# Optimization experiments

Hardware: AMD Instinct MI355X
Metric: run time of the kernel (lower is better)

## Reference

```python
import jax, jax.numpy as jnp
import numpy as np

B, S, H, V = 16, 128, 512, 50000
N, R = 5, 2          # mem_size, read_heads
Wd = H               # memory cell width
EPS = 1e-6
XI_SIZES = [R * Wd, R, Wd, 1, Wd, Wd, R, 1, 1, 3 * R]
XI = int(np.sum(XI_SIZES))  # 2573


def oneplus(x):
    return 1.0 + jax.nn.softplus(x)


def content_weight(M, k, beta):
    # M: [B,N,Wd], k: [B,R,Wd], beta: [B,R] -> [B,R,N]
    Mn = M / (jnp.linalg.norm(M, axis=-1, keepdims=True) + EPS)
    kn = k / (jnp.linalg.norm(k, axis=-1, keepdims=True) + EPS)
    sim = jnp.einsum('brw,bnw->brn', kn, Mn)
    return jax.nn.softmax(beta[:, :, None] * sim, axis=-1)


def setup_inputs() -> dict:
    key = jax.random.key(0)
    ks = jax.random.split(key, 8)
    emb = jax.random.normal(ks[0], (V, H), jnp.float32) * 0.02
    emb = emb.at[0].set(0.0)  # PAD row
    return {
        'source': jax.random.randint(ks[1], (B, S), 0, V),
        'source_lengths': jax.random.randint(ks[2], (B,), 1, S + 1),
        'emb': emb,
        'W_ih': jax.random.normal(ks[3], (4 * H, H + R * Wd), jnp.float32) * 0.02,
        'W_hh': jax.random.normal(ks[4], (4 * H, H), jnp.float32) * 0.02,
        'b_lstm': jnp.zeros((4 * H,), jnp.float32),
        'W_int': jax.random.normal(ks[5], (H, XI), jnp.float32) * 0.02,
        'b_int': jnp.zeros((XI,), jnp.float32),
        'W_out': jax.random.normal(ks[6], (H + R * Wd, H), jnp.float32) * 0.02,
        'b_out': jnp.zeros((H,), jnp.float32),
    }


def dnc_forward(source, emb, W_ih, W_hh, b_lstm, W_int, b_int, W_out, b_out):
    x_emb = emb[source]  # [B,S,H] embedding lookup
    splits = np.cumsum(XI_SIZES)[:-1]
    eye = jnp.eye(N, dtype=jnp.float32)

    def step(carry, x_t):
        h, c, M, u, p, L, wr, ww, r = carry
        # LSTM controller: input = [embedded token; read vectors]
        xin = jnp.concatenate([x_t, r.reshape(-1, R * Wd)], axis=-1)
        gates = xin @ W_ih.T + h @ W_hh.T + b_lstm
        i_, f_, g_, o_ = jnp.split(gates, 4, axis=-1)
        c = jax.nn.sigmoid(f_) * c + jax.nn.sigmoid(i_) * jnp.tanh(g_)
        h = jax.nn.sigmoid(o_) * jnp.tanh(c)
        # interface vector
        xi = h @ W_int + b_int
        (rk, rb, wk, wb, e, v, fg, ga, gw, pi) = jnp.split(xi, splits, axis=-1)
        rk = rk.reshape(-1, R, Wd)
        rb = oneplus(rb)                       # [B,R]
        wb = oneplus(wb)                       # [B,1]
        e = jax.nn.sigmoid(e)                  # [B,Wd]
        fg = jax.nn.sigmoid(fg)                # [B,R]
        ga = jax.nn.sigmoid(ga)                # [B,1]
        gw = jax.nn.sigmoid(gw)                # [B,1]
        pi = jax.nn.softmax(pi.reshape(-1, R, 3), axis=-1)
        # usage / retention
        psi = jnp.prod(1.0 - fg[:, :, None] * wr, axis=1)        # [B,N]
        u = (u + ww - u * ww) * psi
        # allocation weighting (sort-based, irregular access)
        phi = jnp.argsort(u, axis=-1)
        u_s = jnp.take_along_axis(u, phi, axis=-1)
        excl = jnp.concatenate([jnp.ones_like(u_s[:, :1]), jnp.cumprod(u_s, axis=-1)[:, :-1]], axis=-1)
        a_s = (1.0 - u_s) * excl
        a = jnp.take_along_axis(a_s, jnp.argsort(phi, axis=-1), axis=-1)
        # write weighting
        cw = content_weight(M, wk[:, None, :], wb)[:, 0]         # [B,N]
        ww = gw * (ga * a + (1.0 - ga) * cw)
        # memory write
        M = M * (1.0 - ww[:, :, None] * e[:, None, :]) + ww[:, :, None] * v[:, None, :]
        # temporal link matrix + precedence
        L = (1.0 - ww[:, :, None] - ww[:, None, :]) * L + ww[:, :, None] * p[:, None, :]
        L = L * (1.0 - eye)
        p = (1.0 - ww.sum(-1, keepdims=True)) * p + ww
        # read weightings
        fw = jnp.einsum('bij,brj->bri', L, wr)
        bw = jnp.einsum('bji,brj->bri', L, wr)
        cr = content_weight(M, rk, rb)                           # [B,R,N]
        wr = pi[..., 0:1] * bw + pi[..., 1:2] * cr + pi[..., 2:3] * fw
        r = jnp.einsum('brn,bnw->brw', wr, M)                    # [B,R,Wd]
        out_t = jnp.concatenate([h, r.reshape(-1, R * Wd)], axis=-1) @ W_out + b_out
        return (h, c, M, u, p, L, wr, ww, r), out_t

    z = jnp.zeros
    init = (z((B, H)), z((B, H)), z((B, N, Wd)), z((B, N)), z((B, N)),
            z((B, N, N)), z((B, R, N)), z((B, N)), z((B, R, Wd)))
    (h, c, *_), outs = jax.lax.scan(step, init, jnp.swapaxes(x_emb, 0, 1))
    return jnp.swapaxes(outs, 0, 1), h, c


def reference(source, source_lengths, emb, W_ih, W_hh, b_lstm, W_int, b_int, W_out, b_out):
    outputs, h, c = dnc_forward(source, emb, W_ih, W_hh, b_lstm, W_int, b_int, W_out, b_out)
    return outputs, (h, c)
```

## Files before the change

kernel.cpp:

```cpp
#include <hip/hip_runtime.h>
#include <math.h>

#define EPSC 1e-6f
#define NBLK 256
#define GBLK 64

#define OFF_H     0u
#define OFF_R     16384u
#define OFF_FLAGS 32768u
#define OFF_GO    40960u
#define OFF_XF    49152u
#define OFF_RF    57344u
#define STATE_END 58368u
#define OFF_XI    58368u
#define OFF_GX    107520u
#define OFF_HR    4301824u

typedef float f32x4 __attribute__((ext_vector_type(4)));

__device__ __forceinline__ float sigmf(float x) { return 1.0f / (1.0f + expf(-x)); }
__device__ __forceinline__ float oneplusf(float x) {
    return 1.0f + fmaxf(x, 0.0f) + log1pf(expf(-fabsf(x)));
}

__device__ __forceinline__ void gst(float* p, float v) {
    __hip_atomic_store((unsigned*)p, __float_as_uint(v),
                       __ATOMIC_RELAXED, __HIP_MEMORY_SCOPE_AGENT);
}

__device__ __forceinline__ void ld6g(
    f32x4& h0, f32x4& h1,
    f32x4& r0, f32x4& r1, f32x4& r2, f32x4& r3,
    const float* ph, const float* pr)
{
    asm volatile(
        "global_load_dwordx4 %0, %6, off sc0 sc1\n\t"
        "global_load_dwordx4 %1, %6, off offset:1024 sc0 sc1\n\t"
        "global_load_dwordx4 %2, %7, off sc0 sc1\n\t"
        "global_load_dwordx4 %3, %7, off offset:1024 sc0 sc1\n\t"
        "global_load_dwordx4 %4, %7, off offset:2048 sc0 sc1\n\t"
        "global_load_dwordx4 %5, %7, off offset:3072 sc0 sc1\n\t"
        "s_waitcnt vmcnt(0)"
        : "=&v"(h0), "=&v"(h1), "=&v"(r0), "=&v"(r1), "=&v"(r2), "=&v"(r3)
        : "v"(ph), "v"(pr)
        : "memory");
}

__device__ __forceinline__ void ld2h(f32x4& d0, f32x4& d1, const float* p)
{
    asm volatile(
        "global_load_dwordx4 %0, %2, off sc0 sc1\n\t"
        "global_load_dwordx4 %1, %2, off offset:1024 sc0 sc1\n\t"
        "s_waitcnt vmcnt(0)"
        : "=&v"(d0), "=&v"(d1)
        : "v"(p)
        : "memory");
}

__device__ __forceinline__ void cld3(
    f32x4& d0, f32x4& d1, f32x4& d2,
    const float* p0, const float* p1, const float* p2)
{
    asm volatile(
        "global_load_dwordx4 %0, %3, off sc0 sc1\n\t"
        "global_load_dwordx4 %1, %4, off sc0 sc1\n\t"
        "global_load_dwordx4 %2, %5, off sc0 sc1\n\t"
        "s_waitcnt vmcnt(0)"
        : "=&v"(d0), "=&v"(d1), "=&v"(d2)
        : "v"(p0), "v"(p1), "v"(p2)
        : "memory");
}

__device__ __forceinline__ void gsync(unsigned* flags, unsigned* go, unsigned gen,
                                      int bi, int bl, int g, int tid)
{
    __builtin_amdgcn_s_waitcnt(0);
    __syncthreads();
    if (tid == 0)
        __hip_atomic_store(&flags[bi * 32], gen, __ATOMIC_RELAXED, __HIP_MEMORY_SCOPE_AGENT);
    if (bl == 0) {
        if (tid < GBLK) {
            unsigned v;
            do {
                v = __hip_atomic_load(&flags[(g * GBLK + tid) * 32], __ATOMIC_RELAXED,
                                      __HIP_MEMORY_SCOPE_AGENT);
                if (v < gen) __builtin_amdgcn_s_sleep(1);
            } while (v < gen);
        }
        __syncthreads();
        if (tid < GBLK)
            __hip_atomic_store(&go[(g * GBLK + tid) * 32], gen, __ATOMIC_RELAXED,
                               __HIP_MEMORY_SCOPE_AGENT);
    }
    if (tid == 0) {
        unsigned v;
        do {
            v = __hip_atomic_load(&go[bi * 32], __ATOMIC_RELAXED, __HIP_MEMORY_SCOPE_AGENT);
            if (v < gen) __builtin_amdgcn_s_sleep(1);
        } while (v < gen);
    }
    __syncthreads();
}

template <int K>
__device__ __forceinline__ void blk_reduce(float* v, float (*s_red)[20],
                                           float* outp, int tid)
{
#pragma unroll
    for (int i = 0; i < K; i++) {
        float x = v[i];
        for (int o = 32; o > 0; o >>= 1) x += __shfl_down(x, o, 64);
        if ((tid & 63) == 0) s_red[tid >> 6][i] = x;
    }
    __syncthreads();
    if (tid < K) outp[tid] = s_red[0][tid] + s_red[1][tid] + s_red[2][tid] + s_red[3][tid];
    __syncthreads();
}

__global__ __launch_bounds__(256, 1) void k_main(
    const float* __restrict__ W_ih, const float* __restrict__ W_hh,
    const float* __restrict__ W_int, const float* __restrict__ b_int,
    const float* __restrict__ gx, float* __restrict__ hbuf,
    float* __restrict__ rbuf, float* __restrict__ xib,
    float* __restrict__ hr, float* __restrict__ out,
    unsigned* __restrict__ flags, unsigned* __restrict__ go,
    unsigned* __restrict__ xf, unsigned* __restrict__ rf)
{
    const int tid = threadIdx.x;
    const int bi  = blockIdx.x;
    const int g   = bi >> 6;
    const int bl  = bi & 63;
    const int bg0 = g * 4;

    __shared__ __align__(16) float big_u[6656];
    __shared__ __align__(16) float s_xi[3072];
    __shared__ float s_part[512];
    __shared__ float s_tot[128];
    __shared__ float c_s[32];
    __shared__ __align__(16) float s_M[5][520];
    __shared__ float st_u[5], st_p[5], st_L[25], st_wr[10], st_ww[5];
    __shared__ float s_red[4][20];
    __shared__ float s_rb[2], s_wb, s_fg[2], s_ga, s_gw, s_pi[2][3];
    __shared__ float s_wrold[2][5], s_uu[5], s_a[5], s_wwn[5];
    __shared__ float s_pold[5], s_Lnew[25];
    __shared__ float s_zw[5], s_z[2][5], s_fw[2][5], s_bw[2][5];
    __shared__ float s_dotA[11], s_dotB[17], s_wrnew[2][5];

    if (tid < 32) c_s[tid] = 0.f;
    if (bl < 4) {
        for (int i = tid; i < 5 * 520; i += 256) (&s_M[0][0])[i] = 0.f;
        if (tid < 5)  { st_u[tid] = 0.f; st_p[tid] = 0.f; st_ww[tid] = 0.f; }
        if (tid < 25) st_L[tid] = 0.f;
        if (tid < 10) st_wr[tid] = 0.f;
    }
    __syncthreads();

    const int cq = tid & 7;
    const int ks = tid >> 3;
    const int jcol = bl * 8 + cq;
    const int b4 = tid >> 6, sg = tid & 63;

#pragma unroll 1
    for (int t = 0; t < 128; t++) {
        const float* h_in  = hbuf + (t & 1) * 8192;
        float*       h_out = hbuf + ((t + 1) & 1) * 8192;

        float gxv = 0.f;
        if (tid < 128) {
            int c = tid & 31, b = tid >> 5;
            int col = (c >> 3) * 512 + bl * 8 + (c & 7);
            gxv = gx[((size_t)t * 16 + bg0 + b) * 2048 + col];
        }
        if (tid < 4) {
            unsigned v;
            do {
                v = __hip_atomic_load(&rf[(bg0 + tid) * 32], __ATOMIC_RELAXED,
                                      __HIP_MEMORY_SCOPE_AGENT);
                if (v < (unsigned)t) __builtin_amdgcn_s_sleep(4);
            } while (v < (unsigned)t);
        }
        __syncthreads();

        {
            const float* ph = h_in + (bg0 + b4) * 512 + sg * 4;
            const float* pr = rbuf + (bg0 + b4) * 1024 + sg * 4;
            f32x4 h0, h1, r0, r1, r2, r3;
            ld6g(h0, h1, r0, r1, r2, r3, ph, pr);
#define STG(kk, D) { int k = (kk); int cc = k / 48; \
                     *(f32x4*)&big_u[b4 * 1664 + cc * 52 + (k - cc * 48)] = D; }
            STG(sg * 4 + 0 * 256, h0)        STG(sg * 4 + 1 * 256, h1)
            STG(512 + sg * 4 + 0 * 256, r0)  STG(512 + sg * 4 + 1 * 256, r1)
            STG(512 + sg * 4 + 2 * 256, r2)  STG(512 + sg * 4 + 3 * 256, r3)
#undef STG
        }
        __syncthreads();

        float acc[4][4];
#pragma unroll
        for (int g_ = 0; g_ < 4; g_++)
#pragma unroll
            for (int b = 0; b < 4; b++) acc[g_][b] = 0.f;
#pragma unroll
        for (int i = 0; i < 12; i++) {
            int kg = ks * 48 + i * 4;
            f32x4 w[4];
#pragma unroll
            for (int g_ = 0; g_ < 4; g_++) {
                const float* wp = (kg < 512)
                    ? W_hh + (size_t)(g_ * 512 + jcol) * 512 + kg
                    : W_ih + (size_t)(g_ * 512 + jcol) * 1536 + kg;
                w[g_] = *(const f32x4*)wp;
            }
#pragma unroll
            for (int b = 0; b < 4; b++) {
                f32x4 xv = *(const f32x4*)&big_u[b * 1664 + ks * 52 + i * 4];
#pragma unroll
                for (int g_ = 0; g_ < 4; g_++) {
                    acc[g_][b] = fmaf(w[g_][0], xv[0], acc[g_][b]);
                    acc[g_][b] = fmaf(w[g_][1], xv[1], acc[g_][b]);
                    acc[g_][b] = fmaf(w[g_][2], xv[2], acc[g_][b]);
                    acc[g_][b] = fmaf(w[g_][3], xv[3], acc[g_][b]);
                }
            }
        }
#pragma unroll
        for (int g_ = 0; g_ < 4; g_++)
#pragma unroll
            for (int b = 0; b < 4; b++) {
                float x = acc[g_][b];
                x += __shfl_xor(x, 8, 64);
                x += __shfl_xor(x, 16, 64);
                x += __shfl_xor(x, 32, 64);
                acc[g_][b] = x;
            }
        {
            int wv = tid >> 6;
            if ((tid & 63) < 8) {
#pragma unroll
                for (int g_ = 0; g_ < 4; g_++)
#pragma unroll
                    for (int b = 0; b < 4; b++)
                        s_part[((wv * 4 + g_) * 8 + cq) * 4 + b] = acc[g_][b];
            }
        }
        __syncthreads();
        if (tid < 128) {
            int c = tid & 31, b = tid >> 5;
            int g_ = c >> 3, jq = c & 7;
            float tot = gxv;
#pragma unroll
            for (int w = 0; w < 4; w++)
                tot += s_part[((w * 4 + g_) * 8 + jq) * 4 + b];
            s_tot[c * 4 + b] = tot;
        }
        __syncthreads();
        if (tid < 32) {
            int jl = tid & 7, b = tid >> 3;
            float gi  = s_tot[(0 * 8 + jl) * 4 + b];
            float gf  = s_tot[(1 * 8 + jl) * 4 + b];
            float gg  = s_tot[(2 * 8 + jl) * 4 + b];
            float go_ = s_tot[(3 * 8 + jl) * 4 + b];
            float cc = sigmf(gf) * c_s[jl * 4 + b] + sigmf(gi) * tanhf(gg);
            float hh = sigmf(go_) * tanhf(cc);
            c_s[jl * 4 + b] = cc;
            int j = bl * 8 + jl;
            int bgl = bg0 + b;
            gst(h_out + bgl * 512 + j, hh);
            hr[((size_t)t * 16 + bgl) * 1536 + j] = hh;
            if (t == 127) {
                out[1048576 + bgl * 512 + j] = hh;
                out[1048576 + 8192 + bgl * 512 + j] = cc;
            }
        }
        gsync(flags, go, (unsigned)(t + 1), bi, bl, g, tid);

        {
            {
                const float* ph = h_out + (bg0 + b4) * 512 + sg * 4;
                f32x4 e0, e1;
                ld2h(e0, e1, ph);
#define STX(j, E) { int k = sg * 4 + (j) * 256; \
                    *(f32x4*)&big_u[b4 * 592 + (k >> 5) * 36 + (k & 31)] = E; }
                STX(0, e0) STX(1, e1)
#undef STX
            }
            __syncthreads();
            const int ql  = tid & 15;
            const int kcl = tid >> 4;
#pragma unroll 1
            for (int p = 0; p < 3; p++) {
                if (p == 2 && bl >= 33) break;
                int q0 = p * 1024 + bl * 16;
                int q  = q0 + ql;
                int qc = (q < 2573) ? q : 2572;
                float wxr[32];
#pragma unroll
                for (int i = 0; i < 32; i++)
                    wxr[i] = W_int[(size_t)(kcl * 32 + i) * 2573 + qc];
                float ax[4];
#pragma unroll
                for (int b = 0; b < 4; b++) ax[b] = 0.f;
#pragma unroll
                for (int b = 0; b < 4; b++) {
                    const f32x4* hp = (const f32x4*)&big_u[b * 592 + kcl * 36];
#pragma unroll
                    for (int i4 = 0; i4 < 8; i4++) {
                        f32x4 hv = hp[i4];
                        ax[b] = fmaf(wxr[i4 * 4 + 0], hv[0], ax[b]);
                        ax[b] = fmaf(wxr[i4 * 4 + 1], hv[1], ax[b]);
                        ax[b] = fmaf(wxr[i4 * 4 + 2], hv[2], ax[b]);
                        ax[b] = fmaf(wxr[i4 * 4 + 3], hv[3], ax[b]);
                    }
                }
#pragma unroll
                for (int b = 0; b < 4; b++) {
                    float x = ax[b];
                    x += __shfl_xor(x, 16, 64);
                    x += __shfl_xor(x, 32, 64);
                    ax[b] = x;
                }
                {
                    int wv = tid >> 6;
                    if ((tid & 63) < 16) {
#pragma unroll
                        for (int b = 0; b < 4; b++)
                            s_part[(wv * 16 + ql) * 4 + b] = ax[b];
                    }
                }
                __syncthreads();
                if (tid < 64) {
                    int q_l = tid >> 2, b = tid & 3;
                    int qq = q0 + q_l;
                    if (qq < 2573) {
                        float v = b_int[qq];
#pragma unroll
                        for (int w = 0; w < 4; w++)
                            v += s_part[(w * 16 + q_l) * 4 + b];
                        gst(&xib[(bg0 + b) * 3072 + qq], v);
                    }
                }
                __syncthreads();
            }
        }
        __builtin_amdgcn_s_waitcnt(0);
        __syncthreads();
        if (tid == 0)
            __hip_atomic_store(&xf[bi * 32], (unsigned)(t + 1),
                               __ATOMIC_RELAXED, __HIP_MEMORY_SCOPE_AGENT);

        if (bl < 4) {
            const int bg = bg0 + bl;
            if (tid < GBLK) {
                unsigned v;
                do {
                    v = __hip_atomic_load(&xf[(g * GBLK + tid) * 32], __ATOMIC_RELAXED,
                                          __HIP_MEMORY_SCOPE_AGENT);
                    if (v < (unsigned)(t + 1)) __builtin_amdgcn_s_sleep(2);
                } while (v < (unsigned)(t + 1));
            }
            __syncthreads();
            {
                const float* xs = xib + bg * 3072;
                f32x4 d0, d1, d2;
                cld3(d0, d1, d2,
                     xs + (tid + 0) * 4, xs + (tid + 256) * 4, xs + (tid + 512) * 4);
                *(f32x4*)&s_xi[(tid + 0) * 4]   = d0;
                *(f32x4*)&s_xi[(tid + 256) * 4] = d1;
                *(f32x4*)&s_xi[(tid + 512) * 4] = d2;
            }
            __syncthreads();
            const float* xb = s_xi;

            if (tid == 0) {
                s_wb = oneplusf(xb[1538]);
                s_ga = sigmf(xb[2565]);
                s_gw = sigmf(xb[2566]);
            }
            if (tid == 1 || tid == 2) {
                int rr = tid - 1;
                s_rb[rr] = oneplusf(xb[1024 + rr]);
                s_fg[rr] = sigmf(xb[2563 + rr]);
                float z0 = xb[2567 + rr * 3], z1 = xb[2568 + rr * 3], z2 = xb[2569 + rr * 3];
                float mx = fmaxf(z0, fmaxf(z1, z2));
                float e0 = expf(z0 - mx), e1 = expf(z1 - mx), e2 = expf(z2 - mx);
                float s = e0 + e1 + e2;
                s_pi[rr][0] = e0 / s; s_pi[rr][1] = e1 / s; s_pi[rr][2] = e2 / s;
            }
            if (tid >= 32 && tid < 42) { int i = tid - 32; s_wrold[i / 5][i % 5] = st_wr[i]; }
            if (tid >= 64 && tid < 69) { s_pold[tid - 64] = st_p[tid - 64]; }
            __syncthreads();
            if (tid < 5) {
                float psi = (1.f - s_fg[0] * s_wrold[0][tid]) * (1.f - s_fg[1] * s_wrold[1][tid]);
                float un = (st_u[tid] + st_ww[tid] - st_u[tid] * st_ww[tid]) * psi;
                s_uu[tid] = un; st_u[tid] = un;
            }
            __syncthreads();
            if (tid < 5) {
                float excl = 1.f;
#pragma unroll
                for (int m2 = 0; m2 < 5; m2++) {
                    bool before = (s_uu[m2] < s_uu[tid]) || (s_uu[m2] == s_uu[tid] && m2 < tid);
                    if (before) excl *= s_uu[m2];
                }
                s_a[tid] = (1.f - s_uu[tid]) * excl;
            }
            float accA[11];
#pragma unroll
            for (int i = 0; i < 11; i++) accA[i] = 0.f;
            for (int w = tid; w < 512; w += 256) {
                float wk = xb[1026 + w];
                accA[10] += wk * wk;
#pragma unroll
                for (int n = 0; n < 5; n++) {
                    float m_ = s_M[n][w];
                    accA[n]     += m_ * m_;
                    accA[5 + n] += wk * m_;
                }
            }
            blk_reduce<11>(accA, s_red, s_dotA, tid);
            if (tid < 5) {
                float sim = s_dotA[5 + tid] /
                            ((sqrtf(s_dotA[10]) + EPSC) * (sqrtf(s_dotA[tid]) + EPSC));
                s_zw[tid] = s_wb * sim;
            }
            __syncthreads();
            if (tid < 5) {
                float mx = s_zw[0];
#pragma unroll
                for (int m2 = 1; m2 < 5; m2++) mx = fmaxf(mx, s_zw[m2]);
                float sum = 0.f;
#pragma unroll
                for (int m2 = 0; m2 < 5; m2++) sum += expf(s_zw[m2] - mx);
                float cw = expf(s_zw[tid] - mx) / sum;
                float w_ = s_gw * (s_ga * s_a[tid] + (1.f - s_ga) * cw);
                s_wwn[tid] = w_; st_ww[tid] = w_;
            }
            __syncthreads();
            float accB[17];
#pragma unroll
            for (int i = 0; i < 17; i++) accB[i] = 0.f;
            for (int w = tid; w < 512; w += 256) {
                float ew = sigmf(xb[1539 + w]);
                float vw = xb[2051 + w];
                float rk0 = xb[w], rk1 = xb[512 + w];
                accB[15] += rk0 * rk0; accB[16] += rk1 * rk1;
#pragma unroll
                for (int n = 0; n < 5; n++) {
                    float m_ = s_M[n][w];
                    float mn_ = m_ * (1.f - s_wwn[n] * ew) + s_wwn[n] * vw;
                    s_M[n][w] = mn_;
                    accB[n]      += mn_ * mn_;
                    accB[5 + n]  += rk0 * mn_;
                    accB[10 + n] += rk1 * mn_;
                }
            }
            blk_reduce<17>(accB, s_red, s_dotB, tid);
            if (tid < 25) {
                int i2 = tid / 5, j2 = tid % 5;
                float Ln = (i2 == j2) ? 0.f
                         : (1.f - s_wwn[i2] - s_wwn[j2]) * st_L[tid] + s_wwn[i2] * s_pold[j2];
                s_Lnew[tid] = Ln; st_L[tid] = Ln;
            }
            __syncthreads();
            if (tid < 5) {
                float wsum = s_wwn[0] + s_wwn[1] + s_wwn[2] + s_wwn[3] + s_wwn[4];
                st_p[tid] = (1.f - wsum) * s_pold[tid] + s_wwn[tid];
            }
            if (tid < 10) {
                int rr = tid / 5, ii = tid % 5;
                float fw = 0.f, bw = 0.f;
#pragma unroll
                for (int j2 = 0; j2 < 5; j2++) {
                    fw += s_Lnew[ii * 5 + j2] * s_wrold[rr][j2];
                    bw += s_Lnew[j2 * 5 + ii] * s_wrold[rr][j2];
                }
                s_fw[rr][ii] = fw; s_bw[rr][ii] = bw;
                float sim = s_dotB[5 + rr * 5 + ii] /
                            ((sqrtf(s_dotB[15 + rr]) + EPSC) * (sqrtf(s_dotB[ii]) + EPSC));
                s_z[rr][ii] = s_rb[rr] * sim;
            }
            __syncthreads();
            if (tid < 10) {
                int rr = tid / 5, ii = tid % 5;
                float mx = s_z[rr][0];
#pragma unroll
                for (int m2 = 1; m2 < 5; m2++) mx = fmaxf(mx, s_z[rr][m2]);
                float sum = 0.f;
#pragma unroll
                for (int m2 = 0; m2 < 5; m2++) sum += expf(s_z[rr][m2] - mx);
                float cr = expf(s_z[rr][ii] - mx) / sum;
                float wn = s_pi[rr][0] * s_bw[rr][ii] + s_pi[rr][1] * cr + s_pi[rr][2] * s_fw[rr][ii];
                s_wrnew[rr][ii] = wn; st_wr[rr * 5 + ii] = wn;
            }
            __syncthreads();
            for (int idx = tid; idx < 1024; idx += 256) {
                int rr = idx >> 9, w = idx & 511;
                float rv = 0.f;
#pragma unroll
                for (int n = 0; n < 5; n++) rv += s_wrnew[rr][n] * s_M[n][w];
                gst(&rbuf[bg * 1024 + idx], rv);
                hr[((size_t)t * 16 + bg) * 1536 + 512 + idx] = rv;
            }
            __builtin_amdgcn_s_waitcnt(0);
            __syncthreads();
            if (tid == 0)
                __hip_atomic_store(&rf[bg * 32], (unsigned)(t + 1),
                                   __ATOMIC_RELAXED, __HIP_MEMORY_SCOPE_AGENT);
        }
    }
}

__global__ __launch_bounds__(256) void k_embgx(
    const int* __restrict__ src, const float* __restrict__ emb,
    const float* __restrict__ W_ih, const float* __restrict__ b_lstm,
    float* __restrict__ gx)
{
    __shared__ __align__(16) float As[16][68];
    __shared__ __align__(16) float Bs[16][68];
    const int tid = threadIdx.x;
    const int bm = blockIdx.x, bn = blockIdx.y;
    const int tm = tid >> 4, tn = tid & 15;
    float acc[4][4] = {};
    for (int k0 = 0; k0 < 512; k0 += 16) {
#pragma unroll
        for (int i = 0; i < 4; i++) {
            int idx = tid + 256 * i;
            int m = idx >> 4, kk = idx & 15;
            int tok = bm * 64 + m;
            int row = src[(tok & 15) * 128 + (tok >> 4)];
            As[kk][m] = emb[(size_t)row * 512 + k0 + kk];
        }
#pragma unroll
        for (int i = 0; i < 4; i++) {
            int idx = tid + 256 * i;
            int n = idx >> 4, kk = idx & 15;
            Bs[kk][n] = W_ih[(size_t)(bn * 64 + n) * 1536 + k0 + kk];
        }
        __syncthreads();
#pragma unroll
        for (int kk = 0; kk < 16; kk++) {
            float4 av = *(const float4*)&As[kk][tm * 4];
            float4 bv = *(const float4*)&Bs[kk][tn * 4];
            float a[4] = {av.x, av.y, av.z, av.w};
            float b[4] = {bv.x, bv.y, bv.z, bv.w};
#pragma unroll
            for (int i = 0; i < 4; i++)
#pragma unroll
                for (int j = 0; j < 4; j++) acc[i][j] = fmaf(a[i], b[j], acc[i][j]);
        }
        __syncthreads();
    }
#pragma unroll
    for (int i = 0; i < 4; i++) {
        int tok = bm * 64 + tm * 4 + i;
#pragma unroll
        for (int j = 0; j < 4; j++) {
            int col = bn * 64 + tn * 4 + j;
            gx[(size_t)tok * 2048 + col] = acc[i][j] + b_lstm[col];
        }
    }
}

__global__ __launch_bounds__(256) void k_out(
    const float* __restrict__ hr, const float* __restrict__ W_out,
    const float* __restrict__ b_out, float* __restrict__ out)
{
    __shared__ __align__(16) float As[16][68];
    __shared__ __align__(16) float Bs[16][68];
    const int tid = threadIdx.x;
    const int bm = blockIdx.x, bn = blockIdx.y;
    const int tm = tid >> 4, tn = tid & 15;
    float acc[4][4] = {};
    for (int k0 = 0; k0 < 1536; k0 += 16) {
#pragma unroll
        for (int i = 0; i < 4; i++) {
            int idx = tid + 256 * i;
            int m = idx >> 4, kk = idx & 15;
            As[kk][m] = hr[(size_t)(bm * 64 + m) * 1536 + k0 + kk];
        }
#pragma unroll
        for (int i = 0; i < 4; i++) {
            int idx = tid + 256 * i;
            int kk = idx >> 6, n = idx & 63;
            Bs[kk][n] = W_out[(size_t)(k0 + kk) * 512 + bn * 64 + n];
        }
        __syncthreads();
#pragma unroll
        for (int kk = 0; kk < 16; kk++) {
            float4 av = *(const float4*)&As[kk][tm * 4];
            float4 bv = *(const float4*)&Bs[kk][tn * 4];
            float a[4] = {av.x, av.y, av.z, av.w};
            float b[4] = {bv.x, bv.y, bv.z, bv.w};
#pragma unroll
            for (int i = 0; i < 4; i++)
#pragma unroll
                for (int j = 0; j < 4; j++) acc[i][j] = fmaf(a[i], b[j], acc[i][j]);
        }
        __syncthreads();
    }
#pragma unroll
    for (int i = 0; i < 4; i++) {
        int tok = bm * 64 + tm * 4 + i;
        int b_ = tok & 15, s_ = tok >> 4;
#pragma unroll
        for (int j = 0; j < 4; j++) {
            int qn = bn * 64 + tn * 4 + j;
            out[(size_t)((b_ << 7) + s_) * 512 + qn] = acc[i][j] + b_out[qn];
        }
    }
}

extern "C" void kernel_launch(void* const* d_in, const int* in_sizes, int n_in,
                              void* d_out, int out_size, void* d_ws, size_t ws_size,
                              hipStream_t stream)
{
    const int*   src    = (const int*)d_in[0];
    const float* emb    = (const float*)d_in[2];
    const float* W_ih   = (const float*)d_in[3];
    const float* W_hh   = (const float*)d_in[4];
    const float* b_lstm = (const float*)d_in[5];
    const float* W_int  = (const float*)d_in[6];
    const float* b_int  = (const float*)d_in[7];
    const float* W_out  = (const float*)d_in[8];
    const float* b_out  = (const float*)d_in[9];

    float* ws  = (float*)d_ws;
    float* out = (float*)d_out;

    float*    hbuf  = ws + OFF_H;
    float*    rbuf  = ws + OFF_R;
    unsigned* flags = (unsigned*)(ws + OFF_FLAGS);
    unsigned* go    = (unsigned*)(ws + OFF_GO);
    unsigned* xf    = (unsigned*)(ws + OFF_XF);
    unsigned* rf    = (unsigned*)(ws + OFF_RF);
    float*    xib   = ws + OFF_XI;
    float*    gx    = ws + OFF_GX;
    float*    hrb   = ws + OFF_HR;

    hipMemsetAsync(ws, 0, STATE_END * sizeof(float), stream);

    k_embgx<<<dim3(32, 32), 256, 0, stream>>>(src, emb, W_ih, b_lstm, gx);

    k_main<<<dim3(NBLK), dim3(256), 0, stream>>>(
        W_ih, W_hh, W_int, b_int, gx, hbuf, rbuf, xib, hrb, out,
        flags, go, xf, rf);

    k_out<<<dim3(32, 8), 256, 0, stream>>>(hrb, W_out, b_out, out);
}
```

Measured before the change: 3.665 ms.

## Replace two-level group barrier with direct all-to-all flag polling; retile interface matvec

The group barrier, where a leader block gathered flags and then released the others through a go array, becomes a direct scheme: each block posts its flag and then polls all 64 group flags itself. This removes one round trip of cross-block signalling per timestep. The interface-vector matvec is retiled so each thread covers 32 columns with 64 k-values, using two passes instead of three and one fewer shuffle. The rf poll sleep is also shortened. In exchange, flag-polling traffic rises and register pressure grows with the 64-element weight array.

```diff
diff --git a/kernel.cpp b/kernel.cpp
--- a/kernel.cpp
+++ b/kernel.cpp
@@ -7,7 +7,7 @@
 
 #define OFF_H     0u
 #define OFF_R     16384u
-#define OFF_FLAGS 32768u
+#define OFF_HF    32768u
 #define OFF_GO    40960u
 #define OFF_XF    49152u
 #define OFF_RF    57344u
@@ -71,31 +71,21 @@
         : "memory");
 }
 
-__device__ __forceinline__ void gsync(unsigned* flags, unsigned* go, unsigned gen,
-                                      int bi, int bl, int g, int tid)
+__device__ __forceinline__ void post_flag(unsigned* f, unsigned gen, int bi, int tid)
 {
     __builtin_amdgcn_s_waitcnt(0);
     __syncthreads();
     if (tid == 0)
-        __hip_atomic_store(&flags[bi * 32], gen, __ATOMIC_RELAXED, __HIP_MEMORY_SCOPE_AGENT);
-    if (bl == 0) {
-        if (tid < GBLK) {
-            unsigned v;
-            do {
-                v = __hip_atomic_load(&flags[(g * GBLK + tid) * 32], __ATOMIC_RELAXED,
-                                      __HIP_MEMORY_SCOPE_AGENT);
-                if (v < gen) __builtin_amdgcn_s_sleep(1);
-            } while (v < gen);
-        }
-        __syncthreads();
-        if (tid < GBLK)
-            __hip_atomic_store(&go[(g * GBLK + tid) * 32], gen, __ATOMIC_RELAXED,
-                               __HIP_MEMORY_SCOPE_AGENT);
-    }
-    if (tid == 0) {
+        __hip_atomic_store(&f[bi * 32], gen, __ATOMIC_RELAXED, __HIP_MEMORY_SCOPE_AGENT);
+}
+
+__device__ __forceinline__ void wait_flags(unsigned* f, unsigned gen, int g, int tid)
+{
+    if (tid < GBLK) {
         unsigned v;
         do {
-            v = __hip_atomic_load(&go[bi * 32], __ATOMIC_RELAXED, __HIP_MEMORY_SCOPE_AGENT);
+            v = __hip_atomic_load(&f[(g * GBLK + tid) * 32], __ATOMIC_RELAXED,
+                                  __HIP_MEMORY_SCOPE_AGENT);
             if (v < gen) __builtin_amdgcn_s_sleep(1);
         } while (v < gen);
     }
@@ -123,8 +113,8 @@
     const float* __restrict__ gx, float* __restrict__ hbuf,
     float* __restrict__ rbuf, float* __restrict__ xib,
     float* __restrict__ hr, float* __restrict__ out,
-    unsigned* __restrict__ flags, unsigned* __restrict__ go,
-    unsigned* __restrict__ xf, unsigned* __restrict__ rf)
+    unsigned* __restrict__ hf, unsigned* __restrict__ xf,
+    unsigned* __restrict__ rf)
 {
     const int tid = threadIdx.x;
     const int bi  = blockIdx.x;
@@ -159,6 +149,8 @@
     const int ks = tid >> 3;
     const int jcol = bl * 8 + cq;
     const int b4 = tid >> 6, sg = tid & 63;
+    const int xql  = tid & 31;
+    const int xkcl = tid >> 5;
 
 #pragma unroll 1
     for (int t = 0; t < 128; t++) {
@@ -176,7 +168,7 @@
             do {
                 v = __hip_atomic_load(&rf[(bg0 + tid) * 32], __ATOMIC_RELAXED,
                                       __HIP_MEMORY_SCOPE_AGENT);
-                if (v < (unsigned)t) __builtin_amdgcn_s_sleep(4);
+                if (v < (unsigned)t) __builtin_amdgcn_s_sleep(1);
             } while (v < (unsigned)t);
         }
         __syncthreads();
@@ -272,7 +264,8 @@
                 out[1048576 + 8192 + bgl * 512 + j] = cc;
             }
         }
-        gsync(flags, go, (unsigned)(t + 1), bi, bl, g, tid);
+        post_flag(hf, (unsigned)(t + 1), bi, tid);
+        wait_flags(hf, (unsigned)(t + 1), g, tid);
 
         {
             {
@@ -285,80 +278,74 @@
 #undef STX
             }
             __syncthreads();
-            const int ql  = tid & 15;
-            const int kcl = tid >> 4;
 #pragma unroll 1
-            for (int p = 0; p < 3; p++) {
-                if (p == 2 && bl >= 33) break;
-                int q0 = p * 1024 + bl * 16;
-                int q  = q0 + ql;
+            for (int p = 0; p < 2; p++) {
+                if (p == 1 && bl >= 17) break;
+                int q0 = p * 2048 + bl * 32;
+                int q  = q0 + xql;
                 int qc = (q < 2573) ? q : 2572;
-                float wxr[32];
-#pragma unroll
-                for (int i = 0; i < 32; i++)
-                    wxr[i] = W_int[(size_t)(kcl * 32 + i) * 2573 + qc];
+                float wxr[64];
+#pragma unroll
+                for (int i = 0; i < 64; i++)
+                    wxr[i] = W_int[(size_t)(xkcl * 64 + i) * 2573 + qc];
                 float ax[4];
 #pragma unroll
                 for (int b = 0; b < 4; b++) ax[b] = 0.f;
 #pragma unroll
                 for (int b = 0; b < 4; b++) {
-                    const f32x4* hp = (const f32x4*)&big_u[b * 592 + kcl * 36];
+                    const f32x4* hp0 = (const f32x4*)&big_u[b * 592 + (2 * xkcl) * 36];
+                    const f32x4* hp1 = (const f32x4*)&big_u[b * 592 + (2 * xkcl + 1) * 36];
 #pragma unroll
                     for (int i4 = 0; i4 < 8; i4++) {
-                        f32x4 hv = hp[i4];
+                        f32x4 hv = hp0[i4];
                         ax[b] = fmaf(wxr[i4 * 4 + 0], hv[0], ax[b]);
                         ax[b] = fmaf(wxr[i4 * 4 + 1], hv[1], ax[b]);
                         ax[b] = fmaf(wxr[i4 * 4 + 2], hv[2], ax[b]);
                         ax[b] = fmaf(wxr[i4 * 4 + 3], hv[3], ax[b]);
                     }
+#pragma unroll
+                    for (int i4 = 0; i4 < 8; i4++) {
+                        f32x4 hv = hp1[i4];
+                        ax[b] = fmaf(wxr[32 + i4 * 4 + 0], hv[0], ax[b]);
+                        ax[b] = fmaf(wxr[32 + i4 * 4 + 1], hv[1], ax[b]);
+                        ax[b] = fmaf(wxr[32 + i4 * 4 + 2], hv[2], ax[b]);
+                        ax[b] = fmaf(wxr[32 + i4 * 4 + 3], hv[3], ax[b]);
+                    }
                 }
 #pragma unroll
                 for (int b = 0; b < 4; b++) {
                     float x = ax[b];
-                    x += __shfl_xor(x, 16, 64);
                     x += __shfl_xor(x, 32, 64);
                     ax[b] = x;
                 }
                 {
                     int wv = tid >> 6;
-                    if ((tid & 63) < 16) {
+                    if ((tid & 63) < 32) {
 #pragma unroll
                         for (int b = 0; b < 4; b++)
-                            s_part[(wv * 16 + ql) * 4 + b] = ax[b];
+                            s_part[(wv * 32 + xql) * 4 + b] = ax[b];
                     }
                 }
                 __syncthreads();
-                if (tid < 64) {
+                if (tid < 128) {
                     int q_l = tid >> 2, b = tid & 3;
                     int qq = q0 + q_l;
                     if (qq < 2573) {
                         float v = b_int[qq];
 #pragma unroll
                         for (int w = 0; w < 4; w++)
-                            v += s_part[(w * 16 + q_l) * 4 + b];
+                            v += s_part[(w * 32 + q_l) * 4 + b];
                         gst(&xib[(bg0 + b) * 3072 + qq], v);
                     }
                 }
                 __syncthreads();
             }
         }
-        __builtin_amdgcn_s_waitcnt(0);
-        __syncthreads();
-        if (tid == 0)
-            __hip_atomic_store(&xf[bi * 32], (unsigned)(t + 1),
-                               __ATOMIC_RELAXED, __HIP_MEMORY_SCOPE_AGENT);
+        post_flag(xf, (unsigned)(t + 1), bi, tid);
 
         if (bl < 4) {
             const int bg = bg0 + bl;
-            if (tid < GBLK) {
-                unsigned v;
-                do {
-                    v = __hip_atomic_load(&xf[(g * GBLK + tid) * 32], __ATOMIC_RELAXED,
-                                          __HIP_MEMORY_SCOPE_AGENT);
-                    if (v < (unsigned)(t + 1)) __builtin_amdgcn_s_sleep(2);
-                } while (v < (unsigned)(t + 1));
-            }
-            __syncthreads();
+            wait_flags(xf, (unsigned)(t + 1), g, tid);
             {
                 const float* xs = xib + bg * 3072;
                 f32x4 d0, d1, d2;
@@ -501,11 +488,7 @@
                 gst(&rbuf[bg * 1024 + idx], rv);
                 hr[((size_t)t * 16 + bg) * 1536 + 512 + idx] = rv;
             }
-            __builtin_amdgcn_s_waitcnt(0);
-            __syncthreads();
-            if (tid == 0)
-                __hip_atomic_store(&rf[bg * 32], (unsigned)(t + 1),
-                                   __ATOMIC_RELAXED, __HIP_MEMORY_SCOPE_AGENT);
+            post_flag(rf, (unsigned)(t + 1), bg, tid);
         }
     }
 }
@@ -627,15 +610,14 @@
     float* ws  = (float*)d_ws;
     float* out = (float*)d_out;
 
-    float*    hbuf  = ws + OFF_H;
-    float*    rbuf  = ws + OFF_R;
-    unsigned* flags = (unsigned*)(ws + OFF_FLAGS);
-    unsigned* go    = (unsigned*)(ws + OFF_GO);
-    unsigned* xf    = (unsigned*)(ws + OFF_XF);
-    unsigned* rf    = (unsigned*)(ws + OFF_RF);
-    float*    xib   = ws + OFF_XI;
-    float*    gx    = ws + OFF_GX;
-    float*    hrb   = ws + OFF_HR;
+    float*    hbuf = ws + OFF_H;
+    float*    rbuf = ws + OFF_R;
+    unsigned* hf   = (unsigned*)(ws + OFF_HF);
+    unsigned* xf   = (unsigned*)(ws + OFF_XF);
+    unsigned* rf   = (unsigned*)(ws + OFF_RF);
+    float*    xib  = ws + OFF_XI;
+    float*    gx   = ws + OFF_GX;
+    float*    hrb  = ws + OFF_HR;
 
     hipMemsetAsync(ws, 0, STATE_END * sizeof(float), stream);
 
@@ -643,7 +625,7 @@
 
     k_main<<<dim3(NBLK), dim3(256), 0, stream>>>(
         W_ih, W_hh, W_int, b_int, gx, hbuf, rbuf, xib, hrb, out,
-        flags, go, xf, rf);
+        hf, xf, rf);
 
     k_out<<<dim3(32, 8), 256, 0, stream>>>(hrb, W_out, b_out, out);
 }
```

Measured after the change: 3.584 ms. -2.2%, faster.
